# Optimization experiments

Hardware: AMD Instinct MI355X
Metric: run time of the kernel (lower is better)

Reference implementation:

```python
import jax, jax.numpy as jnp
import numpy as np

# channels_choice from the module: [8,16,24,32,40,48,56,64]
CH = jnp.arange(8, 72, 8)
EPS = 1e-5

def _masks():
    # [8,64] binary masks: mask[i, ch] = 1 if ch < channels_choice[i]
    return (jnp.arange(64)[None, :] < CH[:, None]).astype(jnp.float32)

def _bn(x, axes):
    # BatchNorm, affine=False, track_running_stats=False -> batch statistics
    mu = jnp.mean(x, axes, keepdims=True)
    var = jnp.var(x, axes, keepdims=True)
    return (x - mu) * jax.lax.rsqrt(var + EPS)

def _conv3(x, w):
    return jax.lax.conv_general_dilated(x, w, (1, 1), 'SAME',
                                        dimension_numbers=('NCHW', 'OIHW', 'NCHW'))

def _nor_conv(x, w1, w2, a1, a2):
    # Entangled two-part nor_conv edge.
    # p1: relu -> conv3x3 -> bn, mixture over 8 output-channel widths. Slicing
    # output channels + zero-pad + alpha-weighted sum collapses (BN is per-channel)
    # to a soft channel mask m1.
    masks = _masks()                      # [8,64]
    m1 = masks.T @ a1                     # [64] soft output-channel mask
    h = _bn(_conv3(jax.nn.relu(x), w1), (0, 2, 3)) * m1[None, :, None, None]
    # p2: conv3x3 -> bn, mixture over 8 input-channel widths. BN is nonlinear, so
    # the 8 candidates are genuinely computed (vectorized on a leading axis).
    xs = h[None] * masks[:, None, :, None, None]   # [8,B,64,H,W]
    K, B, C, H, W = xs.shape
    y = _conv3(xs.reshape(K * B, C, H, W), w2).reshape(K, B, C, H, W)
    y = _bn(y, (1, 3, 4))
    return jnp.einsum('k,kbchw->bchw', a2, y)

def _avg_pool3(x):
    # AvgPool2d(3, stride=1, padding=1, count_include_pad=False)
    s = jax.lax.reduce_window(x, 0.0, jax.lax.add, (1, 1, 3, 3), (1, 1, 1, 1), 'SAME')
    cnt = jax.lax.reduce_window(jnp.ones((1, 1) + x.shape[2:], x.dtype), 0.0,
                                jax.lax.add, (1, 1, 3, 3), (1, 1, 1, 1), 'SAME')
    return s / cnt

def _combi_mask(a1, a2):
    # combi=True mixture over itertools.product(channels, channels) with weights
    # a1[i]*a2[j]; for channelwise ops (skip/pool) slicing in to c_i then out to c_j
    # keeps channels < min(c_i,c_j), so the double sum factorizes into m1*m2.
    masks = _masks()
    return (masks.T @ a1) * (masks.T @ a2)

def _cell(inputs, alphas1, alphas2, W1_0, W2_0, W1_1, W2_1, W1_4, W2_4, W1_5, W2_5):
    cm = _combi_mask(alphas1, alphas2)[None, :, None, None]
    # genotype: 1<-(conv~0) | 2<-(conv~0, avgpool~1) | 3<-(skip~0, conv~1, conv~2)
    n1 = _nor_conv(inputs, W1_0, W2_0, alphas1, alphas2)
    n2 = _nor_conv(inputs, W1_1, W2_1, alphas1, alphas2) + _avg_pool3(n1) * cm
    n3 = (inputs * cm
          + _nor_conv(n1, W1_4, W2_4, alphas1, alphas2)
          + _nor_conv(n2, W1_5, W2_5, alphas1, alphas2))
    return n3

def setup_inputs():
    key = jax.random.key(0)
    ks = jax.random.split(key, 12)
    B, C, H, W = 64, 64, 32, 32
    a1 = jax.random.uniform(ks[1], (8,), jnp.float32)
    a2 = jax.random.uniform(ks[2], (8,), jnp.float32)
    d = {
        'inputs': jax.random.normal(ks[0], (B, C, H, W), jnp.float32),
        'alphas1': a1 / a1.sum(),
        'alphas2': a2 / a2.sum(),
    }
    wscale = 0.05  # ~ 1/sqrt(64*9) fan-in init
    for i, name in enumerate(['W1_0', 'W2_0', 'W1_1', 'W2_1', 'W1_4', 'W2_4', 'W1_5', 'W2_5']):
        d[name] = jax.random.normal(ks[3 + i], (64, 64, 3, 3), jnp.float32) * wscale
    return d

def reference(inputs, alphas1, alphas2, W1_0, W2_0, W1_1, W2_1, W1_4, W2_4, W1_5, W2_5):
    return _cell(inputs, alphas1, alphas2, W1_0, W2_0, W1_1, W2_1, W1_4, W2_4, W1_5, W2_5)
```

## Files before the change

kernel.cpp:

```cpp
#include <hip/hip_runtime.h>

#define EPS 1e-5f
#define NRED 65536.0f
#define IMST 73984
#define PATCH 8704

typedef short bf16x8 __attribute__((ext_vector_type(8)));
typedef float f32x4 __attribute__((ext_vector_type(4)));
typedef unsigned short u16;

#define MFMA16(a, b, c) __builtin_amdgcn_mfma_f32_16x16x32_bf16(a, b, c, 0, 0, 0)
#define SWZ(px, oct) ((px) * 64 + (((oct) ^ ((px) & 7)) * 8))

__device__ __forceinline__ u16 f2bf(float x) {
  union { float f; unsigned u; } v; v.f = x;
  unsigned r = v.u + 0x7FFF + ((v.u >> 16) & 1);
  return (u16)(r >> 16);
}
__device__ __forceinline__ float bf2f(u16 h) {
  union { unsigned u; float f; } v; v.u = ((unsigned)h) << 16;
  return v.f;
}
__device__ __forceinline__ unsigned pk2(float a, float b) {
  return (unsigned)f2bf(a) | ((unsigned)f2bf(b) << 16);
}

template <int CTRL>
__device__ __forceinline__ float dpp_mov(float x) {
  int xi = __builtin_bit_cast(int, x);
  int r = __builtin_amdgcn_update_dpp(0, xi, CTRL, 0xF, 0xF, true);
  return __builtin_bit_cast(float, r);
}
__device__ __forceinline__ float row_reduce16(float x) {
  x += dpp_mov<0x111>(x);
  x += dpp_mov<0x112>(x);
  x += dpp_mov<0x114>(x);
  x += dpp_mov<0x118>(x);
  return x;
}

__device__ __forceinline__ void stage_mask(const u16* __restrict__ src,
                                           u16* __restrict__ shp, int tid, int R0) {
#pragma unroll
  for (int i = 0; i < 5; ++i) {
    int c = i * 256 + tid;
    if (i == 4 && tid >= 64) break;
    int px = c >> 3, oct = c & 7;
    int prow = px / 34, pcol = px - prow * 34;
    bool halo = (R0 + prow == 0) || (R0 + prow == 33) || (pcol == 0) || (pcol == 33);
    uint4 v = {0u, 0u, 0u, 0u};
    if (!halo) v = *(const uint4*)&src[(size_t)c * 8];
    *(uint4*)&shp[SWZ(px, oct)] = v;
  }
}

__device__ __forceinline__ void stage_affine(const u16* __restrict__ src,
                                             u16* __restrict__ shp, int tid, int R0,
                                             const float* __restrict__ stE) {
  const int oct0 = tid & 7;
  float s[8], bb[8];
#pragma unroll
  for (int j = 0; j < 8; ++j) { s[j] = stE[oct0 * 8 + j]; bb[j] = stE[64 + oct0 * 8 + j]; }
#pragma unroll
  for (int i = 0; i < 5; ++i) {
    int c = i * 256 + tid;
    if (i == 4 && tid >= 64) break;
    int px = c >> 3, oct = c & 7;
    int prow = px / 34, pcol = px - prow * 34;
    bool halo = (R0 + prow == 0) || (R0 + prow == 33) || (pcol == 0) || (pcol == 33);
    uint4 o = {0u, 0u, 0u, 0u};
    if (!halo) {
      uint4 u = *(const uint4*)&src[(size_t)c * 8];
      unsigned uv[4] = {u.x, u.y, u.z, u.w};
      unsigned rv[4];
#pragma unroll
      for (int p2 = 0; p2 < 4; ++p2) {
        float lo = bf2f((u16)(uv[p2] & 0xffff)) * s[p2 * 2] + bb[p2 * 2];
        float hi = bf2f((u16)(uv[p2] >> 16)) * s[p2 * 2 + 1] + bb[p2 * 2 + 1];
        rv[p2] = pk2(lo, hi);
      }
      o.x = rv[0]; o.y = rv[1]; o.z = rv[2]; o.w = rv[3];
    }
    *(uint4*)&shp[SWZ(px, oct)] = o;
  }
}


__global__ void pack_wT1_k(const float* __restrict__ w0, const float* __restrict__ w1,
                           const float* __restrict__ w2, const float* __restrict__ w3,
                           u16* __restrict__ wT1) {
  int e = blockIdx.x / 9, tap = blockIdx.x % 9;
  const float* w = e == 0 ? w0 : e == 1 ? w1 : e == 2 ? w2 : w3;
  u16* dst = wT1 + e * 36864 + tap * 4096;
  for (int idx = threadIdx.x; idx < 4096; idx += 256) {
    int co = idx >> 6, ci = idx & 63;
    dst[idx] = f2bf(w[(co * 64 + ci) * 9 + tap]);
  }
}

__global__ void pack_wG_k(const float* __restrict__ w0, const float* __restrict__ w1,
                          const float* __restrict__ w2, const float* __restrict__ w3,
                          u16* __restrict__ wG64, u16* __restrict__ wT8) {
  int e = blockIdx.y;
  const float* w = e == 0 ? w0 : e == 1 ? w1 : e == 2 ? w2 : w3;
  int bx = blockIdx.x;
  int g, tap;
  u16* dst;
  if (bx < 64) { g = bx >> 3; tap = bx & 7; dst = wG64 + e * 32768 + bx * 512; }
  else         { g = bx - 64; tap = 8;      dst = wT8 + e * 4096 + g * 512; }
  for (int idx = threadIdx.x; idx < 512; idx += 256) {
    int co = idx >> 3, cig = idx & 7;
    dst[idx] = f2bf(w[(co * 64 + g * 8 + cig) * 9 + tap]);
  }
}

__global__ __launch_bounds__(256) void transpose_k(const float* __restrict__ x,
                                                   u16* __restrict__ xT) {
  __shared__ __align__(16) u16 sh[64 * 72];
  const int tid = threadIdx.x;
  const int b = blockIdx.x >> 4, slab = blockIdx.x & 15;
  const int ln = tid & 63, w = tid >> 6;
  const float* xb = x + (size_t)b * 65536 + slab * 64;
#pragma unroll
  for (int i = 0; i < 16; ++i) {
    int ci = w + i * 4;
    float v = xb[ci * 1024 + ln];
    sh[ln * 72 + ci] = f2bf(fmaxf(v, 0.f));
  }
  __syncthreads();
  u16* dst = xT + (size_t)b * IMST;
#pragma unroll
  for (int j = 0; j < 2; ++j) {
    int idx = tid + j * 256;
    int p = idx >> 3, oct = idx & 7;
    int gp = slab * 64 + p;
    int R = gp >> 5, C = gp & 31;
    *(uint4*)&dst[((R + 1) * 34 + C + 1) * 64 + oct * 8] = *(const uint4*)&sh[p * 72 + oct * 8];
  }
}

__global__ void zero_halo_k(u16* __restrict__ buf) {
  int b = blockIdx.x, tid = threadIdx.x;
  if (tid >= 132) return;
  int R, C;
  if (tid < 34) { R = 0; C = tid; }
  else if (tid < 68) { R = 33; C = tid - 34; }
  else if (tid < 100) { R = tid - 67; C = 0; }
  else { R = tid - 99; C = 33; }
  u16* p = buf + (size_t)b * IMST + (size_t)(R * 34 + C) * 64;
  uint4 z = {0u, 0u, 0u, 0u};
#pragma unroll
  for (int i = 0; i < 8; ++i) *(uint4*)&p[i * 8] = z;
}

__global__ __launch_bounds__(256, 2) void convA_k(const u16* __restrict__ in0,
                                                  const u16* __restrict__ in1,
                                                  const u16* __restrict__ wTa,
                                                  const u16* __restrict__ wTb,
                                                  u16* __restrict__ t0,
                                                  u16* __restrict__ t1,
                                                  float* __restrict__ pA) {
  __shared__ __align__(16) u16 shp[PATCH];
  __shared__ float sA[64], qA[64];
  const int tid = threadIdx.x;
  const int b = blockIdx.y, R0 = blockIdx.x * 2, z = blockIdx.z;
  const u16* xin = z ? in1 : in0;
  const u16* wT = z ? wTb : wTa;
  u16* t = z ? t1 : t0;
  if (tid < 64) { sA[tid] = 0.f; qA[tid] = 0.f; }
  stage_mask(xin + (size_t)b * IMST + (size_t)R0 * 2176, shp, tid, R0);
  const int lane = tid & 63, w = tid >> 6;
  const int ln = lane & 15, quad = lane >> 4;
  const int lr = w >> 1, mh = w & 1;
  bf16x8 A[9][2][2];
#pragma unroll
  for (int tap = 0; tap < 9; ++tap)
#pragma unroll
    for (int m2 = 0; m2 < 2; ++m2)
#pragma unroll
      for (int h = 0; h < 2; ++h)
        A[tap][m2][h] = *(const bf16x8*)&wT[(size_t)((tap * 64 + (mh * 2 + m2) * 16 + ln) * 64) + h * 32 + quad * 8];
  __syncthreads();
  f32x4 acc[2][2];
#pragma unroll
  for (int m2 = 0; m2 < 2; ++m2)
#pragma unroll
    for (int nf = 0; nf < 2; ++nf) acc[m2][nf] = (f32x4){0.f, 0.f, 0.f, 0.f};
#pragma unroll
  for (int tap = 0; tap < 9; ++tap) {
    const int dy = tap / 3, dx = tap % 3;
    const int px0 = (lr + dy) * 34 + ln + dx;
#pragma unroll
    for (int h = 0; h < 2; ++h) {
      const int oct = h * 4 + quad;
      bf16x8 b0 = *(const bf16x8*)&shp[SWZ(px0, oct)];
      bf16x8 b1 = *(const bf16x8*)&shp[SWZ(px0 + 16, oct)];
      acc[0][0] = MFMA16(A[tap][0][h], b0, acc[0][0]);
      acc[0][1] = MFMA16(A[tap][0][h], b1, acc[0][1]);
      acc[1][0] = MFMA16(A[tap][1][h], b0, acc[1][0]);
      acc[1][1] = MFMA16(A[tap][1][h], b1, acc[1][1]);
    }
  }
  const int R = R0 + lr;
#pragma unroll
  for (int m2 = 0; m2 < 2; ++m2) {
    const int cob = (mh * 2 + m2) * 16 + quad * 4;
#pragma unroll
    for (int nf = 0; nf < 2; ++nf) {
      u16* tb = t + (size_t)b * IMST + (size_t)((R + 1) * 34 + nf * 16 + ln + 1) * 64 + cob;
      uint2 pk;
      pk.x = pk2(acc[m2][nf][0], acc[m2][nf][1]);
      pk.y = pk2(acc[m2][nf][2], acc[m2][nf][3]);
      *(uint2*)tb = pk;
    }
#pragma unroll
    for (int r = 0; r < 4; ++r) {
      float v0 = acc[m2][0][r], v1 = acc[m2][1][r];
      float s = row_reduce16(v0) + row_reduce16(v1);
      float q = row_reduce16(v0 * v0) + row_reduce16(v1 * v1);
      if (ln == 15) {
        atomicAdd(&sA[cob + r], s);
        atomicAdd(&qA[cob + r], q);
      }
    }
  }
  __syncthreads();
  const int blk = z * 1024 + blockIdx.y * 16 + blockIdx.x;
  if (tid < 64) pA[blk * 128 + tid] = sA[tid];
  else if (tid < 128) pA[blk * 128 + tid] = qA[tid - 64];
}

__global__ __launch_bounds__(256) void reducerA_k(const float* __restrict__ pA,
                                                  const float* __restrict__ a1,
                                                  float* __restrict__ stBase) {
  const int tid = threadIdx.x, c = blockIdx.x, z = blockIdx.y;
  const float* pAe = pA + (size_t)z * 1024 * 128;
  float s = 0.f, q = 0.f;
  for (int i = tid; i < 1024; i += 256) {
    s += pAe[i * 128 + c];
    q += pAe[i * 128 + 64 + c];
  }
#pragma unroll
  for (int off = 32; off; off >>= 1) { s += __shfl_xor(s, off); q += __shfl_xor(q, off); }
  __shared__ float red[8];
  int wv = tid >> 6;
  if ((tid & 63) == 0) { red[wv] = s; red[4 + wv] = q; }
  __syncthreads();
  if (tid == 0) {
    float S = red[0] + red[1] + red[2] + red[3];
    float Q = red[4] + red[5] + red[6] + red[7];
    int g = c >> 3;
    float m = 0.f;
    for (int i = g; i < 8; ++i) m += a1[i];
    float mu = S * (1.f / NRED);
    float var = Q * (1.f / NRED) - mu * mu;
    float r = rsqrtf(var + EPS);
    float* stE = stBase + z * 2048;
    stE[c] = r * m;
    stE[64 + c] = -mu * r * m;
  }
}

__global__ __launch_bounds__(256, 4) void convC_k(const u16* __restrict__ t0,
                                                  const u16* __restrict__ t1,
                                                  const u16* __restrict__ wG64,
                                                  const u16* __restrict__ wT8,
                                                  const float* __restrict__ stBase,
                                                  float* __restrict__ pC) {
  __shared__ __align__(16) u16 shp[PATCH];
  __shared__ __align__(16) u16 shA[64 * 16 * 8];
  __shared__ __align__(16) u16 shA2[8 * 16 * 8];
  __shared__ float sC[128], qC[128];
  const int tid = threadIdx.x;
  const int b = blockIdx.y, R0 = blockIdx.x * 2;
  const int edge = blockIdx.z >> 2, coq = blockIdx.z & 3;
  const u16* t = edge ? t1 : t0;
  const float* stE = stBase + edge * 2048;
  const u16* wGe = wG64 + edge * 32768;
  const u16* wT8e = wT8 + edge * 4096;
  if (tid < 128) { sC[tid] = 0.f; qC[tid] = 0.f; }
  stage_affine(t + (size_t)b * IMST + (size_t)R0 * 2176, shp, tid, R0, stE);
#pragma unroll
  for (int i = 0; i < 4; ++i) {
    int c = i * 256 + tid;
    int row = c >> 4, col = c & 15;
    *(uint4*)&shA[c * 8] = *(const uint4*)&wGe[(size_t)(row * 64 + coq * 16 + col) * 8];
  }
  if (tid < 128) {
    int g = tid >> 4, col = tid & 15;
    *(uint4*)&shA2[tid * 8] = *(const uint4*)&wT8e[(size_t)(g * 64 + coq * 16 + col) * 8];
  }
  __syncthreads();
  const int lane = tid & 63, w = tid >> 6;
  const int ln = lane & 15, quad = lane >> 4;
  const int lrow = w >> 1, colbase = (w & 1) * 16;
  int px[3];
#pragma unroll
  for (int ch = 0; ch < 3; ++ch) {
    int tp = ch * 4 + quad; if (tp > 8) tp = 8;
    px[ch] = (lrow + tp / 3) * 34 + colbase + ln + tp % 3;
  }
  f32x4 acc[8];
#pragma unroll
  for (int g = 0; g < 8; ++g) acc[g] = (f32x4){0.f, 0.f, 0.f, 0.f};
#pragma unroll
  for (int g = 0; g < 8; ++g) {
#pragma unroll
    for (int ch = 0; ch < 3; ++ch) {
      bf16x8 bx = *(const bf16x8*)&shp[SWZ(px[ch], g)];
      bf16x8 aw;
      if (ch < 2) {
        aw = *(const bf16x8*)&shA[((g * 8 + ch * 4 + quad) * 16 + ln) * 8];
      } else {
        aw = (bf16x8){0, 0, 0, 0, 0, 0, 0, 0};
        if (quad == 0) aw = *(const bf16x8*)&shA2[(g * 16 + ln) * 8];
      }
      acc[g] = MFMA16(aw, bx, acc[g]);
    }
  }
  f32x4 P = (f32x4){0.f, 0.f, 0.f, 0.f};
#pragma unroll
  for (int k = 0; k < 8; ++k) {
    P += acc[k];
#pragma unroll
    for (int r = 0; r < 4; ++r) {
      float v = P[r];
      float s = row_reduce16(v);
      float q = row_reduce16(v * v);
      if (ln == 15) {
        atomicAdd(&sC[k * 16 + quad * 4 + r], s);
        atomicAdd(&qC[k * 16 + quad * 4 + r], q);
      }
    }
  }
  __syncthreads();
  const int blk = blockIdx.y * 16 + blockIdx.x;
  const size_t base = ((size_t)(edge * 4 + coq) * 1024 + blk) * 256;
  if (tid < 128) pC[base + tid] = sC[tid];
  else if (tid < 256) pC[base + 128 + (tid - 128)] = qC[tid - 128];
}

__global__ __launch_bounds__(256) void redCprepE_k(const float* __restrict__ pC,
                                                   const float* __restrict__ w2a,
                                                   const float* __restrict__ w2b,
                                                   const float* __restrict__ a1,
                                                   const float* __restrict__ a2,
                                                   float* __restrict__ stBase,
                                                   u16* __restrict__ wEbase,
                                                   float* __restrict__ cm) {
  const int tid = threadIdx.x, c = blockIdx.x, z = blockIdx.y;
  const int coq = c >> 4, cl = c & 15;
  const float* w2 = z ? w2b : w2a;
  float* stE = stBase + z * 2048;
  u16* wE = wEbase + z * 36864;
  float s[8], q[8];
#pragma unroll
  for (int k = 0; k < 8; ++k) { s[k] = 0.f; q[k] = 0.f; }
  for (int i = tid; i < 1024; i += 256) {
    const float* pb = pC + ((size_t)(z * 4 + coq) * 1024 + i) * 256;
#pragma unroll
    for (int k = 0; k < 8; ++k) {
      s[k] += pb[k * 16 + cl];
      q[k] += pb[128 + k * 16 + cl];
    }
  }
#pragma unroll
  for (int k = 0; k < 8; ++k) {
#pragma unroll
    for (int off = 32; off; off >>= 1) { s[k] += __shfl_xor(s[k], off); q[k] += __shfl_xor(q[k], off); }
  }
  __shared__ float red[4][16];
  __shared__ float gL[8];
  int wv = tid >> 6;
  if ((tid & 63) == 0) {
#pragma unroll
    for (int k = 0; k < 8; ++k) { red[wv][k * 2] = s[k]; red[wv][k * 2 + 1] = q[k]; }
  }
  __syncthreads();
  if (tid == 0) {
    float suf = 0.f, bias = 0.f;
    for (int k = 7; k >= 0; --k) {
      float S = red[0][k * 2] + red[1][k * 2] + red[2][k * 2] + red[3][k * 2];
      float Q = red[0][k * 2 + 1] + red[1][k * 2 + 1] + red[2][k * 2 + 1] + red[3][k * 2 + 1];
      float mu = S * (1.f / NRED);
      float var = Q * (1.f / NRED) - mu * mu;
      float rr = rsqrtf(var + EPS);
      bias -= a2[k] * mu * rr;
      suf += a2[k] * rr;
      gL[k] = suf;
    }
    stE[128 + c] = bias;
    if (z == 0) {
      int g = c >> 3;
      float m1 = 0.f, m2 = 0.f;
      for (int i = g; i < 8; ++i) { m1 += a1[i]; m2 += a2[i]; }
      cm[c] = m1 * m2;
    }
  }
  __syncthreads();
  for (int idx = tid; idx < 576; idx += 256) {
    int tap = idx >> 6, ci = idx & 63;
    wE[(tap * 64 + c) * 64 + ci] = f2bf(w2[(c * 64 + ci) * 9 + tap] * gL[ci >> 3]);
  }
}

template <int MODE>
__global__ __launch_bounds__(256, 2) void convE_k(const u16* __restrict__ t,
                                                  const float* __restrict__ stE,
                                                  const u16* __restrict__ wEp,
                                                  u16* __restrict__ d1,
                                                  u16* __restrict__ d2,
                                                  const float* __restrict__ cm) {
  __shared__ __align__(16) u16 shp[PATCH];
  __shared__ float cmL[64], biasL[64];
  const int tid = threadIdx.x;
  const int b = blockIdx.y, R0 = blockIdx.x * 2;
  if (tid < 64) { cmL[tid] = cm[tid]; biasL[tid] = stE[128 + tid]; }
  stage_affine(t + (size_t)b * IMST + (size_t)R0 * 2176, shp, tid, R0, stE);
  const int lane = tid & 63, w = tid >> 6;
  const int ln = lane & 15, quad = lane >> 4;
  const int lr = w >> 1, mh = w & 1;
  bf16x8 A[9][2][2];
#pragma unroll
  for (int tap = 0; tap < 9; ++tap)
#pragma unroll
    for (int m2 = 0; m2 < 2; ++m2)
#pragma unroll
      for (int h = 0; h < 2; ++h)
        A[tap][m2][h] = *(const bf16x8*)&wEp[(size_t)((tap * 64 + (mh * 2 + m2) * 16 + ln) * 64) + h * 32 + quad * 8];
  __syncthreads();
  f32x4 acc[2][2];
#pragma unroll
  for (int m2 = 0; m2 < 2; ++m2)
#pragma unroll
    for (int nf = 0; nf < 2; ++nf) acc[m2][nf] = (f32x4){0.f, 0.f, 0.f, 0.f};
#pragma unroll
  for (int tap = 0; tap < 9; ++tap) {
    const int dy = tap / 3, dx = tap % 3;
    const int px0 = (lr + dy) * 34 + ln + dx;
#pragma unroll
    for (int h = 0; h < 2; ++h) {
      const int oct = h * 4 + quad;
      bf16x8 b0 = *(const bf16x8*)&shp[SWZ(px0, oct)];
      bf16x8 b1 = *(const bf16x8*)&shp[SWZ(px0 + 16, oct)];
      acc[0][0] = MFMA16(A[tap][0][h], b0, acc[0][0]);
      acc[0][1] = MFMA16(A[tap][0][h], b1, acc[0][1]);
      acc[1][0] = MFMA16(A[tap][1][h], b0, acc[1][0]);
      acc[1][1] = MFMA16(A[tap][1][h], b1, acc[1][1]);
    }
  }
  const int R = R0 + lr;
#pragma unroll
  for (int m2 = 0; m2 < 2; ++m2) {
    const int cob = (mh * 2 + m2) * 16 + quad * 4;
#pragma unroll
    for (int nf = 0; nf < 2; ++nf) {
      const int C = nf * 16 + ln;
      const size_t haloPx = (size_t)b * IMST + (size_t)((R + 1) * 34 + C + 1) * 64 + cob;
      float v[4];
#pragma unroll
      for (int r = 0; r < 4; ++r) v[r] = acc[m2][nf][r] + biasL[cob + r];
      if (MODE == 0) {
        uint2 pk, pkr;
        pk.x = pk2(v[0], v[1]); pk.y = pk2(v[2], v[3]);
        pkr.x = pk2(fmaxf(v[0], 0.f), fmaxf(v[1], 0.f));
        pkr.y = pk2(fmaxf(v[2], 0.f), fmaxf(v[3], 0.f));
        *(uint2*)&d1[haloPx] = pk;
        *(uint2*)&d2[haloPx] = pkr;
      } else {
        float ps[4] = {0.f, 0.f, 0.f, 0.f};
        const size_t pb2 = (size_t)b * IMST + (size_t)(R * 34 + C) * 64 + cob;
#pragma unroll
        for (int dy = 0; dy < 3; ++dy)
#pragma unroll
          for (int dx = 0; dx < 3; ++dx) {
            uint2 u = *(const uint2*)&d2[pb2 + (size_t)(dy * 34 + dx) * 64];
            ps[0] += bf2f((u16)(u.x & 0xffff));
            ps[1] += bf2f((u16)(u.x >> 16));
            ps[2] += bf2f((u16)(u.y & 0xffff));
            ps[3] += bf2f((u16)(u.y >> 16));
          }
        float rows = 3.f - (R == 0 ? 1.f : 0.f) - (R == 31 ? 1.f : 0.f);
        float cols = 3.f - (C == 0 ? 1.f : 0.f) - (C == 31 ? 1.f : 0.f);
        float inv = 1.f / (rows * cols);
        uint2 pkr;
        float t0v = fmaxf(v[0] + ps[0] * inv * cmL[cob], 0.f);
        float t1v = fmaxf(v[1] + ps[1] * inv * cmL[cob + 1], 0.f);
        float t2v = fmaxf(v[2] + ps[2] * inv * cmL[cob + 2], 0.f);
        float t3v = fmaxf(v[3] + ps[3] * inv * cmL[cob + 3], 0.f);
        pkr.x = pk2(t0v, t1v); pkr.y = pk2(t2v, t3v);
        *(uint2*)&d1[haloPx] = pkr;
      }
    }
  }
}

__global__ __launch_bounds__(256, 2) void convE23_k(const u16* __restrict__ t0,
                                                    const u16* __restrict__ t1,
                                                    const float* __restrict__ stBase,
                                                    const u16* __restrict__ wE2,
                                                    const u16* __restrict__ wE3,
                                                    float* __restrict__ outp,
                                                    const float* __restrict__ x,
                                                    const float* __restrict__ cm) {
  __shared__ __align__(16) u16 shp2[2 * PATCH];
  __shared__ float cmL[64], biasL[64];
  const int tid = threadIdx.x;
  const int b = blockIdx.y, R0 = blockIdx.x * 2;
  if (tid < 64) {
    cmL[tid] = cm[tid];
    biasL[tid] = stBase[128 + tid] + stBase[2048 + 128 + tid];
  }
  stage_affine(t0 + (size_t)b * IMST + (size_t)R0 * 2176, shp2, tid, R0, stBase);
  stage_affine(t1 + (size_t)b * IMST + (size_t)R0 * 2176, shp2 + PATCH, tid, R0, stBase + 2048);
  __syncthreads();
  const int lane = tid & 63, w = tid >> 6;
  const int ln = lane & 15, quad = lane >> 4;
  const int lr = w >> 1, mh = w & 1;
  f32x4 acc[2][2];
#pragma unroll
  for (int m2 = 0; m2 < 2; ++m2)
#pragma unroll
    for (int nf = 0; nf < 2; ++nf) acc[m2][nf] = (f32x4){0.f, 0.f, 0.f, 0.f};
#pragma unroll 1
  for (int ei = 0; ei < 2; ++ei) {
    const u16* wEp = ei ? wE3 : wE2;
    const u16* sp = &shp2[ei * PATCH];
    bf16x8 A[9][2][2];
#pragma unroll
    for (int tap = 0; tap < 9; ++tap)
#pragma unroll
      for (int m2 = 0; m2 < 2; ++m2)
#pragma unroll
        for (int h = 0; h < 2; ++h)
          A[tap][m2][h] = *(const bf16x8*)&wEp[(size_t)((tap * 64 + (mh * 2 + m2) * 16 + ln) * 64) + h * 32 + quad * 8];
#pragma unroll
    for (int tap = 0; tap < 9; ++tap) {
      const int dy = tap / 3, dx = tap % 3;
      const int px0 = (lr + dy) * 34 + ln + dx;
#pragma unroll
      for (int h = 0; h < 2; ++h) {
        const int oct = h * 4 + quad;
        bf16x8 b0 = *(const bf16x8*)&sp[SWZ(px0, oct)];
        bf16x8 b1 = *(const bf16x8*)&sp[SWZ(px0 + 16, oct)];
        acc[0][0] = MFMA16(A[tap][0][h], b0, acc[0][0]);
        acc[0][1] = MFMA16(A[tap][0][h], b1, acc[0][1]);
        acc[1][0] = MFMA16(A[tap][1][h], b0, acc[1][0]);
        acc[1][1] = MFMA16(A[tap][1][h], b1, acc[1][1]);
      }
    }
  }
  const int R = R0 + lr;
#pragma unroll
  for (int m2 = 0; m2 < 2; ++m2) {
    const int cob = (mh * 2 + m2) * 16 + quad * 4;
#pragma unroll
    for (int nf = 0; nf < 2; ++nf) {
      const int C = nf * 16 + ln;
      size_t base = (size_t)b * 65536 + (size_t)cob * 1024 + R * 32 + C;
#pragma unroll
      for (int r = 0; r < 4; ++r)
        outp[base + (size_t)r * 1024] =
            acc[m2][nf][r] + biasL[cob + r] + x[base + (size_t)r * 1024] * cmL[cob + r];
    }
  }
}

extern "C" void kernel_launch(void* const* d_in, const int* in_sizes, int n_in,
                              void* d_out, int out_size, void* d_ws, size_t ws_size,
                              hipStream_t stream) {
  const float* x  = (const float*)d_in[0];
  const float* a1 = (const float*)d_in[1];
  const float* a2 = (const float*)d_in[2];
  const float* W1[4] = {(const float*)d_in[3], (const float*)d_in[5],
                        (const float*)d_in[7], (const float*)d_in[9]};
  const float* W2[4] = {(const float*)d_in[4], (const float*)d_in[6],
                        (const float*)d_in[8], (const float*)d_in[10]};
  float* out = (float*)d_out;
  char* ws = (char*)d_ws;
  const size_t HB = (size_t)IMST * 64 * 2;
  u16* xT  = (u16*)ws;
  u16* t0  = (u16*)(ws + HB);
  u16* t1  = (u16*)(ws + 2 * HB);
  u16* n1T = (u16*)(ws + 3 * HB);
  u16* n1r = (u16*)(ws + 4 * HB);
  u16* n2r = (u16*)(ws + 5 * HB);
  char* p = ws + 6 * HB;
  float* st  = (float*)p;            p += 8256 * 4;
  u16* wT1   = (u16*)p;              p += 4 * 36864 * 2;
  u16* wG64  = (u16*)p;              p += 4 * 32768 * 2;
  u16* wT8   = (u16*)p;              p += 4 * 4096 * 2;
  u16* wE    = (u16*)p;              p += 4 * 36864 * 2;
  float* pA  = (float*)p;            p += 2 * 1024 * 128 * 4;
  float* pC  = (float*)p;
  float* cm  = st + 8192;

  pack_wT1_k<<<36, 256, 0, stream>>>(W1[0], W1[1], W1[2], W1[3], wT1);
  pack_wG_k<<<dim3(72, 4), 256, 0, stream>>>(W2[0], W2[1], W2[2], W2[3], wG64, wT8);
  transpose_k<<<1024, 256, 0, stream>>>(x, xT);
  zero_halo_k<<<64, 160, 0, stream>>>(n1T);

  dim3 gA(16, 64, 2), gC(16, 64, 8), gE(16, 64);
  convA_k<<<gA, 256, 0, stream>>>(xT, xT, wT1, wT1 + 36864, t0, t1, pA);
  reducerA_k<<<dim3(64, 2), 256, 0, stream>>>(pA, a1, st);
  convC_k<<<gC, 256, 0, stream>>>(t0, t1, wG64, wT8, st, pC);
  redCprepE_k<<<dim3(64, 2), 256, 0, stream>>>(pC, W2[0], W2[1], a1, a2, st, wE, cm);
  convE_k<0><<<gE, 256, 0, stream>>>(t0, st, wE, n1T, n1r, cm);
  convE_k<1><<<gE, 256, 0, stream>>>(t1, st + 2048, wE + 36864, n2r, n1T, cm);
  convA_k<<<gA, 256, 0, stream>>>(n1r, n2r, wT1 + 2 * 36864, wT1 + 3 * 36864, t0, t1, pA);
  reducerA_k<<<dim3(64, 2), 256, 0, stream>>>(pA, a1, st + 4096);
  convC_k<<<gC, 256, 0, stream>>>(t0, t1, wG64 + 2 * 32768, wT8 + 2 * 4096, st + 4096, pC);
  redCprepE_k<<<dim3(64, 2), 256, 0, stream>>>(pC, W2[2], W2[3], a1, a2, st + 4096,
                                               wE + 2 * 36864, cm);
  convE23_k<<<gE, 256, 0, stream>>>(t0, t1, st + 4096, wE + 2 * 36864, wE + 3 * 36864,
                                    out, x, cm);
}
```

Before: 466.3 us.

## Loop over output-channel quarters inside convC to reuse staged input patch

convC now processes all four output-channel quarters in one block, looping over them and reloading only the weight tiles, so the affine-transformed input patch is staged once per block rather than four times. The grid shrinks from 8 to 2 in z, which cuts redundant global reads and affine work. In exchange there are four times fewer blocks, extra barriers between serialized weight reloads, and more shared memory for the per-quarter statistics.

```diff
diff --git a/kernel.cpp b/kernel.cpp
--- a/kernel.cpp
+++ b/kernel.cpp
@@ -270,25 +270,30 @@
   __shared__ __align__(16) u16 shp[PATCH];
   __shared__ __align__(16) u16 shA[64 * 16 * 8];
   __shared__ __align__(16) u16 shA2[8 * 16 * 8];
-  __shared__ float sC[128], qC[128];
+  __shared__ float sC[4][128], qC[4][128];
   const int tid = threadIdx.x;
   const int b = blockIdx.y, R0 = blockIdx.x * 2;
-  const int edge = blockIdx.z >> 2, coq = blockIdx.z & 3;
+  const int edge = blockIdx.z;
   const u16* t = edge ? t1 : t0;
   const float* stE = stBase + edge * 2048;
   const u16* wGe = wG64 + edge * 32768;
   const u16* wT8e = wT8 + edge * 4096;
-  if (tid < 128) { sC[tid] = 0.f; qC[tid] = 0.f; }
+  {
+    float* scf = (float*)sC;
+    float* qcf = (float*)qC;
+#pragma unroll
+    for (int i = 0; i < 2; ++i) { scf[i * 256 + tid] = 0.f; qcf[i * 256 + tid] = 0.f; }
+  }
   stage_affine(t + (size_t)b * IMST + (size_t)R0 * 2176, shp, tid, R0, stE);
 #pragma unroll
   for (int i = 0; i < 4; ++i) {
     int c = i * 256 + tid;
     int row = c >> 4, col = c & 15;
-    *(uint4*)&shA[c * 8] = *(const uint4*)&wGe[(size_t)(row * 64 + coq * 16 + col) * 8];
+    *(uint4*)&shA[c * 8] = *(const uint4*)&wGe[(size_t)(row * 64 + col) * 8];
   }
   if (tid < 128) {
     int g = tid >> 4, col = tid & 15;
-    *(uint4*)&shA2[tid * 8] = *(const uint4*)&wT8e[(size_t)(g * 64 + coq * 16 + col) * 8];
+    *(uint4*)&shA2[tid * 8] = *(const uint4*)&wT8e[(size_t)(g * 64 + col) * 8];
   }
   __syncthreads();
   const int lane = tid & 63, w = tid >> 6;
@@ -300,44 +305,64 @@
     int tp = ch * 4 + quad; if (tp > 8) tp = 8;
     px[ch] = (lrow + tp / 3) * 34 + colbase + ln + tp % 3;
   }
-  f32x4 acc[8];
-#pragma unroll
-  for (int g = 0; g < 8; ++g) acc[g] = (f32x4){0.f, 0.f, 0.f, 0.f};
-#pragma unroll
-  for (int g = 0; g < 8; ++g) {
-#pragma unroll
-    for (int ch = 0; ch < 3; ++ch) {
-      bf16x8 bx = *(const bf16x8*)&shp[SWZ(px[ch], g)];
-      bf16x8 aw;
-      if (ch < 2) {
-        aw = *(const bf16x8*)&shA[((g * 8 + ch * 4 + quad) * 16 + ln) * 8];
-      } else {
-        aw = (bf16x8){0, 0, 0, 0, 0, 0, 0, 0};
-        if (quad == 0) aw = *(const bf16x8*)&shA2[(g * 16 + ln) * 8];
-      }
-      acc[g] = MFMA16(aw, bx, acc[g]);
-    }
-  }
-  f32x4 P = (f32x4){0.f, 0.f, 0.f, 0.f};
-#pragma unroll
-  for (int k = 0; k < 8; ++k) {
-    P += acc[k];
-#pragma unroll
-    for (int r = 0; r < 4; ++r) {
-      float v = P[r];
-      float s = row_reduce16(v);
-      float q = row_reduce16(v * v);
-      if (ln == 15) {
-        atomicAdd(&sC[k * 16 + quad * 4 + r], s);
-        atomicAdd(&qC[k * 16 + quad * 4 + r], q);
-      }
-    }
-  }
-  __syncthreads();
+#pragma unroll 1
+  for (int coq = 0; coq < 4; ++coq) {
+    f32x4 acc[8];
+#pragma unroll
+    for (int g = 0; g < 8; ++g) acc[g] = (f32x4){0.f, 0.f, 0.f, 0.f};
+#pragma unroll
+    for (int g = 0; g < 8; ++g) {
+#pragma unroll
+      for (int ch = 0; ch < 3; ++ch) {
+        bf16x8 bx = *(const bf16x8*)&shp[SWZ(px[ch], g)];
+        bf16x8 aw;
+        if (ch < 2) {
+          aw = *(const bf16x8*)&shA[((g * 8 + ch * 4 + quad) * 16 + ln) * 8];
+        } else {
+          aw = (bf16x8){0, 0, 0, 0, 0, 0, 0, 0};
+          if (quad == 0) aw = *(const bf16x8*)&shA2[(g * 16 + ln) * 8];
+        }
+        acc[g] = MFMA16(aw, bx, acc[g]);
+      }
+    }
+    f32x4 P = (f32x4){0.f, 0.f, 0.f, 0.f};
+#pragma unroll
+    for (int k = 0; k < 8; ++k) {
+      P += acc[k];
+#pragma unroll
+      for (int r = 0; r < 4; ++r) {
+        float v = P[r];
+        float s = row_reduce16(v);
+        float q = row_reduce16(v * v);
+        if (ln == 15) {
+          atomicAdd(&sC[coq][k * 16 + quad * 4 + r], s);
+          atomicAdd(&qC[coq][k * 16 + quad * 4 + r], q);
+        }
+      }
+    }
+    __syncthreads();
+    if (coq < 3) {
+      const int nq = coq + 1;
+#pragma unroll
+      for (int i = 0; i < 4; ++i) {
+        int c = i * 256 + tid;
+        int row = c >> 4, col = c & 15;
+        *(uint4*)&shA[c * 8] = *(const uint4*)&wGe[(size_t)(row * 64 + nq * 16 + col) * 8];
+      }
+      if (tid < 128) {
+        int g = tid >> 4, col = tid & 15;
+        *(uint4*)&shA2[tid * 8] = *(const uint4*)&wT8e[(size_t)(g * 64 + nq * 16 + col) * 8];
+      }
+      __syncthreads();
+    }
+  }
   const int blk = blockIdx.y * 16 + blockIdx.x;
-  const size_t base = ((size_t)(edge * 4 + coq) * 1024 + blk) * 256;
-  if (tid < 128) pC[base + tid] = sC[tid];
-  else if (tid < 256) pC[base + 128 + (tid - 128)] = qC[tid - 128];
+#pragma unroll 1
+  for (int coq = 0; coq < 4; ++coq) {
+    const size_t base = ((size_t)(edge * 4 + coq) * 1024 + blk) * 256;
+    if (tid < 128) pC[base + tid] = sC[coq][tid];
+    else pC[base + 128 + (tid - 128)] = qC[coq][tid - 128];
+  }
 }
 
 __global__ __launch_bounds__(256) void redCprepE_k(const float* __restrict__ pC,
@@ -600,7 +625,7 @@
   transpose_k<<<1024, 256, 0, stream>>>(x, xT);
   zero_halo_k<<<64, 160, 0, stream>>>(n1T);
 
-  dim3 gA(16, 64, 2), gC(16, 64, 8), gE(16, 64);
+  dim3 gA(16, 64, 2), gC(16, 64, 2), gE(16, 64);
   convA_k<<<gA, 256, 0, stream>>>(xT, xT, wT1, wT1 + 36864, t0, t1, pA);
   reducerA_k<<<dim3(64, 2), 256, 0, stream>>>(pA, a1, st);
   convC_k<<<gC, 256, 0, stream>>>(t0, t1, wG64, wT8, st, pC);
```

New measurement: 466.2 us. Within noise of the previous version (-0.0%).

## Make convC blocks persistent over four row pairs with register-prefetched patches

Applied to the files above, without the earlier changes.

Each convC block now handles 8 output rows in four 2-row steps instead of 2 rows, cutting the grid by 4x. The next patch is prefetched into registers while the current MFMA step runs, and the affine transform is applied when writing to shared memory. Per-step sums and sums of squares are kept in registers and reduced once at the end, which shrinks partial-stat writes and the matching read loop in redCprepE. The trade-offs are more registers (launch bounds lowered from 4 to 3), two barriers per step, and fewer blocks to fill the GPU.

```diff
diff --git a/kernel.cpp b/kernel.cpp
--- a/kernel.cpp
+++ b/kernel.cpp
@@ -261,7 +261,7 @@
   }
 }
 
-__global__ __launch_bounds__(256, 4) void convC_k(const u16* __restrict__ t0,
+__global__ __launch_bounds__(256, 3) void convC_k(const u16* __restrict__ t0,
                                                   const u16* __restrict__ t1,
                                                   const u16* __restrict__ wG64,
                                                   const u16* __restrict__ wT8,
@@ -272,14 +272,33 @@
   __shared__ __align__(16) u16 shA2[8 * 16 * 8];
   __shared__ float sC[128], qC[128];
   const int tid = threadIdx.x;
-  const int b = blockIdx.y, R0 = blockIdx.x * 2;
+  const int b = blockIdx.y, R0 = blockIdx.x * 8;
   const int edge = blockIdx.z >> 2, coq = blockIdx.z & 3;
   const u16* t = edge ? t1 : t0;
   const float* stE = stBase + edge * 2048;
   const u16* wGe = wG64 + edge * 32768;
   const u16* wT8e = wT8 + edge * 4096;
+  const u16* src = t + (size_t)b * IMST;
   if (tid < 128) { sC[tid] = 0.f; qC[tid] = 0.f; }
-  stage_affine(t + (size_t)b * IMST + (size_t)R0 * 2176, shp, tid, R0, stE);
+  const int oct0 = tid & 7;
+  float sc[8], bc[8];
+#pragma unroll
+  for (int j = 0; j < 8; ++j) { sc[j] = stE[oct0 * 8 + j]; bc[j] = stE[64 + oct0 * 8 + j]; }
+  uint4 ld[5];
+  int hmask = 0;
+#pragma unroll
+  for (int i = 0; i < 5; ++i) {
+    int c = i * 256 + tid;
+    uint4 v = {0u, 0u, 0u, 0u};
+    if (!(i == 4 && tid >= 64)) {
+      int px = c >> 3;
+      int prow = px / 34, pcol = px - prow * 34;
+      bool halo = (R0 + prow == 0) || (R0 + prow == 33) || (pcol == 0) || (pcol == 33);
+      if (!halo) v = *(const uint4*)&src[(size_t)(R0 * 2176) + (size_t)c * 8];
+      if (halo) hmask |= 1 << i;
+    } else hmask |= 1 << i;
+    ld[i] = v;
+  }
 #pragma unroll
   for (int i = 0; i < 4; ++i) {
     int c = i * 256 + tid;
@@ -290,7 +309,6 @@
     int g = tid >> 4, col = tid & 15;
     *(uint4*)&shA2[tid * 8] = *(const uint4*)&wT8e[(size_t)(g * 64 + coq * 16 + col) * 8];
   }
-  __syncthreads();
   const int lane = tid & 63, w = tid >> 6;
   const int ln = lane & 15, quad = lane >> 4;
   const int lrow = w >> 1, colbase = (w & 1) * 16;
@@ -300,44 +318,92 @@
     int tp = ch * 4 + quad; if (tp > 8) tp = 8;
     px[ch] = (lrow + tp / 3) * 34 + colbase + ln + tp % 3;
   }
-  f32x4 acc[8];
-#pragma unroll
-  for (int g = 0; g < 8; ++g) acc[g] = (f32x4){0.f, 0.f, 0.f, 0.f};
-#pragma unroll
-  for (int g = 0; g < 8; ++g) {
-#pragma unroll
-    for (int ch = 0; ch < 3; ++ch) {
-      bf16x8 bx = *(const bf16x8*)&shp[SWZ(px[ch], g)];
-      bf16x8 aw;
-      if (ch < 2) {
-        aw = *(const bf16x8*)&shA[((g * 8 + ch * 4 + quad) * 16 + ln) * 8];
-      } else {
-        aw = (bf16x8){0, 0, 0, 0, 0, 0, 0, 0};
-        if (quad == 0) aw = *(const bf16x8*)&shA2[(g * 16 + ln) * 8];
-      }
-      acc[g] = MFMA16(aw, bx, acc[g]);
-    }
-  }
-  f32x4 P = (f32x4){0.f, 0.f, 0.f, 0.f};
+  f32x4 sL[8], qL[8];
+#pragma unroll
+  for (int k = 0; k < 8; ++k) { sL[k] = (f32x4){0.f, 0.f, 0.f, 0.f}; qL[k] = (f32x4){0.f, 0.f, 0.f, 0.f}; }
+#pragma unroll 1
+  for (int tau = 0; tau < 4; ++tau) {
+#pragma unroll
+    for (int i = 0; i < 5; ++i) {
+      if (i == 4 && tid >= 64) break;
+      int c = i * 256 + tid;
+      int ppx = c >> 3, oct = c & 7;
+      uint4 o = {0u, 0u, 0u, 0u};
+      if (!((hmask >> i) & 1)) {
+        unsigned uv[4] = {ld[i].x, ld[i].y, ld[i].z, ld[i].w};
+        unsigned rv[4];
+#pragma unroll
+        for (int p2 = 0; p2 < 4; ++p2) {
+          float lo = bf2f((u16)(uv[p2] & 0xffff)) * sc[p2 * 2] + bc[p2 * 2];
+          float hi = bf2f((u16)(uv[p2] >> 16)) * sc[p2 * 2 + 1] + bc[p2 * 2 + 1];
+          rv[p2] = pk2(lo, hi);
+        }
+        o.x = rv[0]; o.y = rv[1]; o.z = rv[2]; o.w = rv[3];
+      }
+      *(uint4*)&shp[SWZ(ppx, oct)] = o;
+    }
+    __syncthreads();
+    if (tau < 3) {
+      const int Rn = R0 + 2 * (tau + 1);
+      hmask = 0;
+#pragma unroll
+      for (int i = 0; i < 5; ++i) {
+        int c = i * 256 + tid;
+        uint4 v = {0u, 0u, 0u, 0u};
+        if (!(i == 4 && tid >= 64)) {
+          int ppx = c >> 3;
+          int prow = ppx / 34, pcol = ppx - prow * 34;
+          bool halo = (Rn + prow == 0) || (Rn + prow == 33) || (pcol == 0) || (pcol == 33);
+          if (!halo) v = *(const uint4*)&src[(size_t)(Rn * 2176) + (size_t)c * 8];
+          if (halo) hmask |= 1 << i;
+        } else hmask |= 1 << i;
+        ld[i] = v;
+      }
+    }
+    f32x4 acc[8];
+#pragma unroll
+    for (int g = 0; g < 8; ++g) acc[g] = (f32x4){0.f, 0.f, 0.f, 0.f};
+#pragma unroll
+    for (int g = 0; g < 8; ++g) {
+#pragma unroll
+      for (int ch = 0; ch < 3; ++ch) {
+        bf16x8 bx = *(const bf16x8*)&shp[SWZ(px[ch], g)];
+        bf16x8 aw;
+        if (ch < 2) {
+          aw = *(const bf16x8*)&shA[((g * 8 + ch * 4 + quad) * 16 + ln) * 8];
+        } else {
+          aw = (bf16x8){0, 0, 0, 0, 0, 0, 0, 0};
+          if (quad == 0) aw = *(const bf16x8*)&shA2[(g * 16 + ln) * 8];
+        }
+        acc[g] = MFMA16(aw, bx, acc[g]);
+      }
+    }
+    f32x4 P = (f32x4){0.f, 0.f, 0.f, 0.f};
+#pragma unroll
+    for (int k = 0; k < 8; ++k) {
+      P += acc[k];
+      sL[k] += P;
+      qL[k] += P * P;
+    }
+    __syncthreads();
+  }
 #pragma unroll
   for (int k = 0; k < 8; ++k) {
-    P += acc[k];
 #pragma unroll
     for (int r = 0; r < 4; ++r) {
-      float v = P[r];
-      float s = row_reduce16(v);
-      float q = row_reduce16(v * v);
+      float ss = row_reduce16(sL[k][r]);
+      float qq = row_reduce16(qL[k][r]);
       if (ln == 15) {
-        atomicAdd(&sC[k * 16 + quad * 4 + r], s);
-        atomicAdd(&qC[k * 16 + quad * 4 + r], q);
-      }
-    }
-  }
-  __syncthreads();
-  const int blk = blockIdx.y * 16 + blockIdx.x;
-  const size_t base = ((size_t)(edge * 4 + coq) * 1024 + blk) * 256;
+        atomicAdd(&sC[k * 16 + quad * 4 + r], ss);
+        atomicAdd(&qC[k * 16 + quad * 4 + r], qq);
+      }
+    }
+  }
+  __syncthreads();
+  const int blk = blockIdx.y * 4 + blockIdx.x;
+  const size_t base = ((size_t)(edge * 4 + coq) * 256 + blk) * 256;
   if (tid < 128) pC[base + tid] = sC[tid];
-  else if (tid < 256) pC[base + 128 + (tid - 128)] = qC[tid - 128];
+  else pC[base + 128 + (tid - 128)] = qC[tid - 128];
 }
 
 __global__ __launch_bounds__(256) void redCprepE_k(const float* __restrict__ pC,
@@ -356,8 +422,8 @@
   float s[8], q[8];
 #pragma unroll
   for (int k = 0; k < 8; ++k) { s[k] = 0.f; q[k] = 0.f; }
-  for (int i = tid; i < 1024; i += 256) {
-    const float* pb = pC + ((size_t)(z * 4 + coq) * 1024 + i) * 256;
+  for (int i = tid; i < 256; i += 256) {
+    const float* pb = pC + ((size_t)(z * 4 + coq) * 256 + i) * 256;
 #pragma unroll
     for (int k = 0; k < 8; ++k) {
       s[k] += pb[k * 16 + cl];
@@ -600,7 +666,7 @@
   transpose_k<<<1024, 256, 0, stream>>>(x, xT);
   zero_halo_k<<<64, 160, 0, stream>>>(n1T);
 
-  dim3 gA(16, 64, 2), gC(16, 64, 8), gE(16, 64);
+  dim3 gA(16, 64, 2), gC(4, 64, 8), gE(16, 64);
   convA_k<<<gA, 256, 0, stream>>>(xT, xT, wT1, wT1 + 36864, t0, t1, pA);
   reducerA_k<<<dim3(64, 2), 256, 0, stream>>>(pA, a1, st);
   convC_k<<<gC, 256, 0, stream>>>(t0, t1, wG64, wT8, st, pC);
```

After: 495.5 us. 6.3% more time.
